# Performance work log

Measured on AMD Instinct MI355X. Metric: run time of the kernel, lower is better.

Reference implementation:

```python
import jax, jax.numpy as jnp
import numpy as np

E = 1024  # hidden_size
H = 16    # num_heads
D = E // H  # head_dim = 64


def setup_inputs() -> dict:
    key = jax.random.key(0)
    ks = jax.random.split(key, 10)
    s = 1.0 / np.sqrt(E)
    inp = {
        "hidden_states": jax.random.normal(ks[0], (2, 2048, E), dtype=jnp.float32),
        "attention_mask": jnp.ones((2, 2048), dtype=jnp.float32),
        "Wq": jax.random.normal(ks[1], (E, E), dtype=jnp.float32) * s,
        "bq": jnp.zeros((E,), dtype=jnp.float32),
        "Wk": jax.random.normal(ks[2], (E, E), dtype=jnp.float32) * s,
        "bk": jnp.zeros((E,), dtype=jnp.float32),
        "Wv": jax.random.normal(ks[3], (E, E), dtype=jnp.float32) * s,
        "bv": jnp.zeros((E,), dtype=jnp.float32),
        "Wo": jax.random.normal(ks[4], (E, E), dtype=jnp.float32) * s,
        "bo": jnp.zeros((E,), dtype=jnp.float32),
    }
    return inp


def _split_heads(x):
    # [B, S, E] -> [B, H, S, D]
    b, s, _ = x.shape
    return x.reshape(b, s, H, D).transpose(0, 2, 1, 3)


def reference(hidden_states, attention_mask, Wq, bq, Wk, bk, Wv, bv, Wo, bo):
    b, s, _ = hidden_states.shape
    q = _split_heads(hidden_states @ Wq + bq)  # [B,H,S,D]
    k = _split_heads(hidden_states @ Wk + bk)
    v = _split_heads(hidden_states @ Wv + bv)
    scores = jnp.einsum('bhqd,bhkd->bhqk', q, k) / jnp.sqrt(jnp.float32(D))
    scores = scores + (1.0 - attention_mask)[:, None, None, :] * -10000.0
    probs = jax.nn.softmax(scores, axis=-1)
    ctx = jnp.einsum('bhqk,bhkd->bhqd', probs, v)  # [B,H,S,D]
    ctx = ctx.transpose(0, 2, 1, 3).reshape(b, s, E)
    return ctx @ Wo + bo
```

## Files before the change

kernel.cpp:

```cpp
#include <hip/hip_runtime.h>
#include <hip/hip_bf16.h>
#include <stdint.h>

typedef __bf16 bf16x8 __attribute__((ext_vector_type(8)));
typedef __bf16 bf16x4_t __attribute__((ext_vector_type(4)));
typedef float  f32x4  __attribute__((ext_vector_type(4)));
typedef short  short8 __attribute__((ext_vector_type(8)));
typedef short  short4v __attribute__((ext_vector_type(4)));
typedef float  float4v __attribute__((ext_vector_type(4)));

#define AS1 __attribute__((address_space(1)))
#define AS3 __attribute__((address_space(3)))

__device__ __forceinline__ void g2l16(const void* g, void* l) {
    __builtin_amdgcn_global_load_lds((const AS1 void*)g, (AS3 void*)l, 16, 0, 0);
}

__device__ __forceinline__ short f2bf(float f) {
    unsigned u = __builtin_bit_cast(unsigned, f);
    unsigned r = u + 0x7FFFu + ((u >> 16) & 1u);
    return (short)(r >> 16);
}

__device__ __forceinline__ bf16x8 ldb8(const short* p) {
    return __builtin_bit_cast(bf16x8, *(const short8*)p);
}

__device__ __forceinline__ float fast_exp2(float x) {
    return __builtin_amdgcn_exp2f(x);
}

#define LOG2E 1.44269504f
#define QSCL (0.125f * LOG2E)

__global__ __launch_bounds__(256) void cast_x(const float* __restrict__ X,
                                              short* __restrict__ Xb) {
    int i = (blockIdx.x * 256 + threadIdx.x) * 4;
    float4v v = *(const float4v*)(X + i);
    short4v o;
    o[0] = f2bf(v[0]); o[1] = f2bf(v[1]); o[2] = f2bf(v[2]); o[3] = f2bf(v[3]);
    *(short4v*)(Xb + i) = o;
}

__global__ __launch_bounds__(256) void transpose_w(
    const float* __restrict__ W0, const float* __restrict__ W1,
    const float* __restrict__ W2, const float* __restrict__ W3,
    short* __restrict__ T0, short* __restrict__ T1,
    short* __restrict__ T2, short* __restrict__ T3) {
    int z = blockIdx.z;
    const float* W = z == 0 ? W0 : z == 1 ? W1 : z == 2 ? W2 : W3;
    short* T = z == 0 ? T0 : z == 1 ? T1 : z == 2 ? T2 : T3;
    __shared__ float t[32][33];
    int n0 = blockIdx.x * 32, k0 = blockIdx.y * 32;
    int tx = threadIdx.x & 31, ty = threadIdx.x >> 5;
#pragma unroll
    for (int i = 0; i < 4; i++)
        t[ty + i * 8][tx] = W[(size_t)(k0 + ty + i * 8) * 1024 + n0 + tx];
    __syncthreads();
#pragma unroll
    for (int i = 0; i < 4; i++)
        T[(size_t)(n0 + ty + i * 8) * 1024 + k0 + tx] = f2bf(t[tx][ty + i * 8]);
}

__global__ __launch_bounds__(256) void gemm_qkv(
    const short* __restrict__ Xb,
    const short* __restrict__ WqT, const short* __restrict__ WkT, const short* __restrict__ WvT,
    const float* __restrict__ bq, const float* __restrict__ bk, const float* __restrict__ bv,
    short* __restrict__ Qb, short* __restrict__ Kb, short* __restrict__ VT) {
    const int K = 1024, N = 1024;
    int mt = blockIdx.x;
    int yy = blockIdx.y;
    int mat = yy >> 3, nt = yy & 7;
    const short* Bt = mat == 0 ? WqT : mat == 1 ? WkT : WvT;
    const float* bias = mat == 0 ? bq : mat == 1 ? bk : bv;

    int tid = threadIdx.x;
    int w = tid >> 6, lane = tid & 63;
    int quad = lane >> 4, l16 = lane & 15;
    int wy = w >> 1, wx = w & 1;

    __shared__ __align__(16) short A_lds[128 * 32];
    __shared__ __align__(16) short B_lds[128 * 32];

    f32x4 acc[4][4];
#pragma unroll
    for (int mi = 0; mi < 4; mi++)
#pragma unroll
        for (int ni = 0; ni < 4; ni++) acc[mi][ni] = (f32x4){0.f, 0.f, 0.f, 0.f};

    int m0 = mt * 128, n0 = nt * 128;
    for (int kt = 0; kt < 32; kt++) {
        __syncthreads();
#pragma unroll
        for (int c = 0; c < 2; c++) {
            int row = w * 32 + c * 16 + (lane >> 2);
            g2l16(Xb + (size_t)(m0 + row) * K + kt * 32 + (lane & 3) * 8,
                  &A_lds[(w * 32 + c * 16) * 32]);
            g2l16(Bt + (size_t)(n0 + row) * K + kt * 32 + (lane & 3) * 8,
                  &B_lds[(w * 32 + c * 16) * 32]);
        }
        __syncthreads();
        bf16x8 af[4], bfr[4];
#pragma unroll
        for (int i = 0; i < 4; i++) {
            af[i]  = ldb8(&A_lds[(wy * 64 + i * 16 + l16) * 32 + quad * 8]);
            bfr[i] = ldb8(&B_lds[(wx * 64 + i * 16 + l16) * 32 + quad * 8]);
        }
#pragma unroll
        for (int mi = 0; mi < 4; mi++)
#pragma unroll
            for (int ni = 0; ni < 4; ni++)
                acc[mi][ni] = __builtin_amdgcn_mfma_f32_16x16x32_bf16(af[mi], bfr[ni], acc[mi][ni], 0, 0, 0);
    }

    if (mat < 2) {
        short* Cout = mat == 0 ? Qb : Kb;
        float s = mat == 0 ? QSCL : 1.0f;
#pragma unroll
        for (int ni = 0; ni < 4; ni++) {
            int col = n0 + wx * 64 + ni * 16 + l16;
            float bv_ = bias[col];
#pragma unroll
            for (int mi = 0; mi < 4; mi++)
#pragma unroll
                for (int r = 0; r < 4; r++) {
                    int row = m0 + wy * 64 + mi * 16 + quad * 4 + r;
                    Cout[(size_t)row * N + col] = f2bf((acc[mi][ni][r] + bv_) * s);
                }
        }
    } else {
#pragma unroll
        for (int ni = 0; ni < 4; ni++) {
            int col = n0 + wx * 64 + ni * 16 + l16;
            float bv_ = bias[col];
#pragma unroll
            for (int mi = 0; mi < 4; mi++) {
                int row0 = m0 + wy * 64 + mi * 16 + quad * 4;
                int bb = row0 >> 11, ss = row0 & 2047;
                f32x4 a = acc[mi][ni];
                f32x4 av = {a[0] + bv_, a[1] + bv_, a[2] + bv_, a[3] + bv_};
                bf16x4_t ob = __builtin_convertvector(av, bf16x4_t);
                *(short4v*)&VT[((size_t)(bb * 16) << 17) + ((size_t)col * 2048) + ss] =
                    __builtin_bit_cast(short4v, ob);
            }
        }
    }
}

__global__ __launch_bounds__(256) void gemm_out(
    const short* __restrict__ Ab, const short* __restrict__ Bt,
    const float* __restrict__ bias, float* __restrict__ C) {
    const int K = 1024, N = 1024;
    int mt = blockIdx.x, nt = blockIdx.y;
    int tid = threadIdx.x;
    int w = tid >> 6, lane = tid & 63;
    int quad = lane >> 4, l16 = lane & 15;

    __shared__ __align__(16) short A_lds[64 * 32];
    __shared__ __align__(16) short B_lds[128 * 32];

    f32x4 acc[4][2];
#pragma unroll
    for (int mi = 0; mi < 4; mi++)
#pragma unroll
        for (int ni = 0; ni < 2; ni++) acc[mi][ni] = (f32x4){0.f, 0.f, 0.f, 0.f};

    int m0 = mt * 64, n0 = nt * 128;
    for (int kt = 0; kt < 32; kt++) {
        __syncthreads();
        {
            int row = w * 16 + (lane >> 2);
            g2l16(Ab + (size_t)(m0 + row) * K + kt * 32 + (lane & 3) * 8,
                  &A_lds[(w * 16) * 32]);
        }
#pragma unroll
        for (int c = 0; c < 2; c++) {
            int row = w * 32 + c * 16 + (lane >> 2);
            g2l16(Bt + (size_t)(n0 + row) * K + kt * 32 + (lane & 3) * 8,
                  &B_lds[(w * 32 + c * 16) * 32]);
        }
        __syncthreads();
        bf16x8 af[4], bfr[2];
#pragma unroll
        for (int i = 0; i < 4; i++)
            af[i] = ldb8(&A_lds[(i * 16 + l16) * 32 + quad * 8]);
#pragma unroll
        for (int i = 0; i < 2; i++)
            bfr[i] = ldb8(&B_lds[(w * 32 + i * 16 + l16) * 32 + quad * 8]);
#pragma unroll
        for (int mi = 0; mi < 4; mi++)
#pragma unroll
            for (int ni = 0; ni < 2; ni++)
                acc[mi][ni] = __builtin_amdgcn_mfma_f32_16x16x32_bf16(af[mi], bfr[ni], acc[mi][ni], 0, 0, 0);
    }
#pragma unroll
    for (int ni = 0; ni < 2; ni++) {
        int col = n0 + w * 32 + ni * 16 + l16;
        float bv_ = bias[col];
#pragma unroll
        for (int mi = 0; mi < 4; mi++)
#pragma unroll
            for (int r = 0; r < 4; r++) {
                int row = m0 + mi * 16 + quad * 4 + r;
                C[(size_t)row * N + col] = acc[mi][ni][r] + bv_;
            }
    }
}

#define PROW 72
__global__ __launch_bounds__(512) void attn_kernel(
    const short* __restrict__ Qb, const short* __restrict__ Kb,
    const short* __restrict__ VT, const float* __restrict__ mask,
    short* __restrict__ ctx) {
    const int S = 2048, E = 1024, HH = 16;
    int qb = blockIdx.x;
    int h = blockIdx.y;
    int b = blockIdx.z;
    int tid = threadIdx.x;
    int w = tid >> 6, lane = tid & 63;
    int quad = lane >> 4, l16 = lane & 15;

    __shared__ __align__(16) short K_lds[64 * 64];
    __shared__ __align__(16) short VT_lds[64 * 64];
    __shared__ __align__(16) short P_lds[8][16 * PROW];
    __shared__ int maskflag;

    if (tid == 0) maskflag = 1;
    __syncthreads();
    {
        float4v m = *(const float4v*)(mask + b * S + tid * 4);
        if (!(m[0] == 1.f && m[1] == 1.f && m[2] == 1.f && m[3] == 1.f))
            maskflag = 0;
    }
    __syncthreads();
    const bool nomask = (maskflag != 0);

    int q0 = qb * 128;

    bf16x8 qf[2];
#pragma unroll
    for (int kc = 0; kc < 2; kc++)
        qf[kc] = ldb8(Qb + (size_t)(b * S + q0 + w * 16 + l16) * E + h * 64 + kc * 32 + quad * 8);

    f32x4 O_t[4];
    float mstate = -1e30f, lstate = 0.f;
#pragma unroll
    for (int nd = 0; nd < 4; nd++) O_t[nd] = (f32x4){0.f, 0.f, 0.f, 0.f};

    const short* Kbase = Kb + (size_t)b * S * E + h * 64;
    const short* Vbase = VT + (size_t)(b * HH + h) * 64 * S;
    short* Pw = &P_lds[w][0];
    int rsw = l16 & 7;

    for (int kt = 0; kt < 32; kt++) {
        int k0 = kt * 64;
        __syncthreads();
        {
            int row = w * 8 + (lane >> 3);
            int srcb = (lane & 7) ^ (row & 7);
            g2l16(Kbase + (size_t)(k0 + row) * E + srcb * 8, &K_lds[(w * 8) * 64]);
            g2l16(Vbase + (size_t)row * S + k0 + srcb * 8, &VT_lds[(w * 8) * 64]);
        }
        __syncthreads();

        f32x4 sc[4];
#pragma unroll
        for (int ni = 0; ni < 4; ni++) sc[ni] = (f32x4){0.f, 0.f, 0.f, 0.f};
#pragma unroll
        for (int ni = 0; ni < 4; ni++) {
#pragma unroll
            for (int kc = 0; kc < 2; kc++) {
                int blk = (kc * 4 + quad) ^ rsw;
                bf16x8 kf = ldb8(&K_lds[(ni * 16 + l16) * 64 + blk * 8]);
                sc[ni] = __builtin_amdgcn_mfma_f32_16x16x32_bf16(kf, qf[kc], sc[ni], 0, 0, 0);
            }
        }

        if (!nomask) {
#pragma unroll
            for (int ni = 0; ni < 4; ni++) {
                float4v mrow = *(const float4v*)(mask + b * S + k0 + ni * 16 + quad * 4);
#pragma unroll
                for (int r = 0; r < 4; r++)
                    sc[ni][r] += (1.0f - mrow[r]) * (-10000.0f * LOG2E);
            }
        }

        float mx = sc[0][0];
#pragma unroll
        for (int ni = 0; ni < 4; ni++)
#pragma unroll
            for (int r = 0; r < 4; r++) mx = fmaxf(mx, sc[ni][r]);
        mx = fmaxf(mx, __shfl_xor(mx, 16, 64));
        mx = fmaxf(mx, __shfl_xor(mx, 32, 64));

        float newm = fmaxf(mstate, mx);
        float alpha = fast_exp2(mstate - newm);
        mstate = newm;

        float rs = 0.f;
#pragma unroll
        for (int ni = 0; ni < 4; ni++)
#pragma unroll
            for (int r = 0; r < 4; r++) {
                float p = fast_exp2(sc[ni][r] - newm);
                sc[ni][r] = p;
                rs += p;
            }
        rs += __shfl_xor(rs, 16, 64);
        rs += __shfl_xor(rs, 32, 64);
        lstate = lstate * alpha + rs;
#pragma unroll
        for (int nd = 0; nd < 4; nd++)
#pragma unroll
            for (int r = 0; r < 4; r++) O_t[nd][r] *= alpha;

#pragma unroll
        for (int ni = 0; ni < 4; ni++) {
            bf16x4_t pb = __builtin_convertvector(sc[ni], bf16x4_t);
            *(short4v*)&Pw[l16 * PROW + ni * 16 + quad * 4] =
                __builtin_bit_cast(short4v, pb);
        }

#pragma unroll
        for (int ks = 0; ks < 2; ks++) {
            bf16x8 pf = ldb8(&Pw[l16 * PROW + ks * 32 + quad * 8]);
#pragma unroll
            for (int nd = 0; nd < 4; nd++) {
                int blk = (ks * 4 + quad) ^ rsw;
                bf16x8 vf = ldb8(&VT_lds[(nd * 16 + l16) * 64 + blk * 8]);
                O_t[nd] = __builtin_amdgcn_mfma_f32_16x16x32_bf16(vf, pf, O_t[nd], 0, 0, 0);
            }
        }
    }

    {
        float l = lstate;
        float inv = l > 0.f ? 1.0f / l : 0.f;
        int row = q0 + w * 16 + l16;
#pragma unroll
        for (int nd = 0; nd < 4; nd++) {
            f32x4 o = O_t[nd];
            f32x4 os = {o[0] * inv, o[1] * inv, o[2] * inv, o[3] * inv};
            bf16x4_t ob = __builtin_convertvector(os, bf16x4_t);
            *(short4v*)&ctx[(size_t)(b * S + row) * E + h * 64 + nd * 16 + quad * 4] =
                __builtin_bit_cast(short4v, ob);
        }
    }
}

extern "C" void kernel_launch(void* const* d_in, const int* in_sizes, int n_in,
                              void* d_out, int out_size, void* d_ws, size_t ws_size,
                              hipStream_t stream) {
    const float* X    = (const float*)d_in[0];
    const float* mask = (const float*)d_in[1];
    const float* Wq   = (const float*)d_in[2];
    const float* bq   = (const float*)d_in[3];
    const float* Wk   = (const float*)d_in[4];
    const float* bk   = (const float*)d_in[5];
    const float* Wv   = (const float*)d_in[6];
    const float* bv   = (const float*)d_in[7];
    const float* Wo   = (const float*)d_in[8];
    const float* bo   = (const float*)d_in[9];
    float* out = (float*)d_out;

    char* ws = (char*)d_ws;
    short* Xb  = (short*)(ws);
    short* WqT = (short*)(ws + (8u << 20));
    short* WkT = (short*)(ws + (10u << 20));
    short* WvT = (short*)(ws + (12u << 20));
    short* WoT = (short*)(ws + (14u << 20));
    short* Qb  = (short*)(ws + (16u << 20));
    short* Kb  = (short*)(ws + (24u << 20));
    short* VT  = (short*)(ws + (32u << 20));
    short* ctx = Xb;

    cast_x<<<4096, 256, 0, stream>>>(X, Xb);
    transpose_w<<<dim3(32, 32, 4), 256, 0, stream>>>(Wq, Wk, Wv, Wo, WqT, WkT, WvT, WoT);
    gemm_qkv<<<dim3(32, 24), 256, 0, stream>>>(Xb, WqT, WkT, WvT, bq, bk, bv, Qb, Kb, VT);
    attn_kernel<<<dim3(16, 16, 2), 512, 0, stream>>>(Qb, Kb, VT, mask, ctx);
    gemm_out<<<dim3(64, 8), 256, 0, stream>>>(ctx, WoT, bo, out);
}
```

Baseline: 219.8 us.

## Stage V transpose through LDS and shrink attention blocks with remapped grid

The V-projection epilogue now writes results into shared memory and then emits coalesced 16-byte rows of the transposed V buffer, replacing scattered 8-byte stores. The attention kernel drops from 512 threads with 128 queries per block to 256 threads with 64 queries per block. It runs on a 1D grid of 1024 blocks whose index mapping groups 8 (batch, head) pairs together, which should help K/V cache reuse and doubles the block count. In exchange, each K/V tile is loaded from global memory by twice as many blocks.

```diff
diff --git a/kernel.cpp b/kernel.cpp
--- a/kernel.cpp
+++ b/kernel.cpp
@@ -62,6 +62,7 @@
         T[(size_t)(n0 + ty + i * 8) * 1024 + k0 + tx] = f2bf(t[tx][ty + i * 8]);
 }
 
+#define VROW 136
 __global__ __launch_bounds__(256) void gemm_qkv(
     const short* __restrict__ Xb,
     const short* __restrict__ WqT, const short* __restrict__ WkT, const short* __restrict__ WvT,
@@ -79,8 +80,9 @@
     int quad = lane >> 4, l16 = lane & 15;
     int wy = w >> 1, wx = w & 1;
 
-    __shared__ __align__(16) short A_lds[128 * 32];
-    __shared__ __align__(16) short B_lds[128 * 32];
+    __shared__ __align__(16) short smem[128 * VROW];
+    short* A_lds = smem;
+    short* B_lds = smem + 4096;
 
     f32x4 acc[4][4];
 #pragma unroll
@@ -129,20 +131,29 @@
                 }
         }
     } else {
+        __syncthreads();
 #pragma unroll
         for (int ni = 0; ni < 4; ni++) {
-            int col = n0 + wx * 64 + ni * 16 + l16;
-            float bv_ = bias[col];
+            int cl = wx * 64 + ni * 16 + l16;
+            float bv_ = bias[n0 + cl];
 #pragma unroll
             for (int mi = 0; mi < 4; mi++) {
-                int row0 = m0 + wy * 64 + mi * 16 + quad * 4;
-                int bb = row0 >> 11, ss = row0 & 2047;
+                int ml = wy * 64 + mi * 16 + quad * 4;
                 f32x4 a = acc[mi][ni];
                 f32x4 av = {a[0] + bv_, a[1] + bv_, a[2] + bv_, a[3] + bv_};
                 bf16x4_t ob = __builtin_convertvector(av, bf16x4_t);
-                *(short4v*)&VT[((size_t)(bb * 16) << 17) + ((size_t)col * 2048) + ss] =
-                    __builtin_bit_cast(short4v, ob);
-            }
+                *(short4v*)&smem[cl * VROW + ml] = __builtin_bit_cast(short4v, ob);
+            }
+        }
+        __syncthreads();
+        int bb = m0 >> 11, ss0 = m0 & 2047;
+        int t16 = tid & 15, cw = tid >> 4;
+#pragma unroll
+        for (int p = 0; p < 8; p++) {
+            int cl = p * 16 + cw;
+            int col = n0 + cl;
+            *(short8*)&VT[(((size_t)(bb * 16)) << 17) + (size_t)col * 2048 + ss0 + t16 * 8] =
+                *(const short8*)&smem[cl * VROW + t16 * 8];
         }
     }
 }
@@ -208,34 +219,39 @@
 }
 
 #define PROW 72
-__global__ __launch_bounds__(512) void attn_kernel(
+__global__ __launch_bounds__(256) void attn_kernel(
     const short* __restrict__ Qb, const short* __restrict__ Kb,
     const short* __restrict__ VT, const float* __restrict__ mask,
     short* __restrict__ ctx) {
     const int S = 2048, E = 1024, HH = 16;
-    int qb = blockIdx.x;
-    int h = blockIdx.y;
-    int b = blockIdx.z;
+    int g = blockIdx.x;
+    int low = g & 7, k = g >> 3;
+    int p = low + 8 * (k >> 5);
+    int qb = k & 31;
+    int b = p >> 4, h = p & 15;
+
     int tid = threadIdx.x;
     int w = tid >> 6, lane = tid & 63;
     int quad = lane >> 4, l16 = lane & 15;
 
     __shared__ __align__(16) short K_lds[64 * 64];
     __shared__ __align__(16) short VT_lds[64 * 64];
-    __shared__ __align__(16) short P_lds[8][16 * PROW];
+    __shared__ __align__(16) short P_lds[4][16 * PROW];
     __shared__ int maskflag;
 
     if (tid == 0) maskflag = 1;
     __syncthreads();
     {
-        float4v m = *(const float4v*)(mask + b * S + tid * 4);
-        if (!(m[0] == 1.f && m[1] == 1.f && m[2] == 1.f && m[3] == 1.f))
+        float4v m0 = *(const float4v*)(mask + b * S + tid * 8);
+        float4v m1 = *(const float4v*)(mask + b * S + tid * 8 + 4);
+        if (!(m0[0] == 1.f && m0[1] == 1.f && m0[2] == 1.f && m0[3] == 1.f &&
+              m1[0] == 1.f && m1[1] == 1.f && m1[2] == 1.f && m1[3] == 1.f))
             maskflag = 0;
     }
     __syncthreads();
     const bool nomask = (maskflag != 0);
 
-    int q0 = qb * 128;
+    int q0 = qb * 64;
 
     bf16x8 qf[2];
 #pragma unroll
@@ -255,11 +271,12 @@
     for (int kt = 0; kt < 32; kt++) {
         int k0 = kt * 64;
         __syncthreads();
-        {
-            int row = w * 8 + (lane >> 3);
+#pragma unroll
+        for (int c = 0; c < 2; c++) {
+            int row = w * 16 + c * 8 + (lane >> 3);
             int srcb = (lane & 7) ^ (row & 7);
-            g2l16(Kbase + (size_t)(k0 + row) * E + srcb * 8, &K_lds[(w * 8) * 64]);
-            g2l16(Vbase + (size_t)row * S + k0 + srcb * 8, &VT_lds[(w * 8) * 64]);
+            g2l16(Kbase + (size_t)(k0 + row) * E + srcb * 8, &K_lds[(w * 16 + c * 8) * 64]);
+            g2l16(Vbase + (size_t)row * S + k0 + srcb * 8, &VT_lds[(w * 16 + c * 8) * 64]);
         }
         __syncthreads();
 
@@ -303,9 +320,9 @@
         for (int ni = 0; ni < 4; ni++)
 #pragma unroll
             for (int r = 0; r < 4; r++) {
-                float p = fast_exp2(sc[ni][r] - newm);
-                sc[ni][r] = p;
-                rs += p;
+                float pp = fast_exp2(sc[ni][r] - newm);
+                sc[ni][r] = pp;
+                rs += pp;
             }
         rs += __shfl_xor(rs, 16, 64);
         rs += __shfl_xor(rs, 32, 64);
@@ -378,6 +395,6 @@
     cast_x<<<4096, 256, 0, stream>>>(X, Xb);
     transpose_w<<<dim3(32, 32, 4), 256, 0, stream>>>(Wq, Wk, Wv, Wo, WqT, WkT, WvT, WoT);
     gemm_qkv<<<dim3(32, 24), 256, 0, stream>>>(Xb, WqT, WkT, WvT, bq, bk, bv, Qb, Kb, VT);
-    attn_kernel<<<dim3(16, 16, 2), 512, 0, stream>>>(Qb, Kb, VT, mask, ctx);
+    attn_kernel<<<1024, 256, 0, stream>>>(Qb, Kb, VT, mask, ctx);
     gemm_out<<<dim3(64, 8), 256, 0, stream>>>(ctx, WoT, bo, out);
 }
```

Measured after the change: 225.6 us. +2.7%, slower.
